# Optimization experiments

Hardware: AMD Instinct MI355X
Metric: run time of the kernel (lower is better)

Reference implementation:

```python
import jax, jax.numpy as jnp
import numpy as np
from jax import lax

B, S, D = 4, 2048, 256      # batch, seq_len, hidden_dim
F = 1024                    # ffn_dim
E = 32                      # num_experts
K = 4                       # top_k


def setup_inputs() -> dict:
    key = jax.random.key(0)
    ks = jax.random.split(key, 5)
    scale = 0.02
    x = jax.random.normal(ks[0], (B, S, D), dtype=jnp.float32)
    router_w = jax.random.normal(ks[1], (E, D), dtype=jnp.float32) * scale   # gate Linear weight [out=E, in=D]
    w_gate = jax.random.normal(ks[2], (E, F, D), dtype=jnp.float32) * scale  # per-expert [F, D]
    w_up = jax.random.normal(ks[3], (E, F, D), dtype=jnp.float32) * scale
    w_down = jax.random.normal(ks[4], (E, D, F), dtype=jnp.float32) * scale
    return {"x": x, "router_w": router_w, "w_gate": w_gate, "w_up": w_up, "w_down": w_down}


def reference(x, router_w, w_gate, w_up, w_down):
    # Eval mode: jitter noise and dropout are inactive (training-only in the source).
    b, s, d = x.shape
    T = b * s
    xf = x.reshape(T, d)                                   # [T, D]

    # --- Router ---
    logits = xf @ router_w.T                               # [T, E]
    tk_logits, tk_idx = lax.top_k(logits, K)               # [T, K]
    tk_w = jax.nn.softmax(tk_logits, axis=-1)              # [T, K]
    probs = jax.nn.softmax(logits, axis=-1)                # [T, E]
    one_hot = jax.nn.one_hot(tk_idx, E, dtype=x.dtype)     # [T, K, E]
    tokens_per_expert = one_hot.sum(axis=(0, 1))           # [E]
    f_frac = tokens_per_expert / T
    P = probs.mean(axis=0)
    aux_loss = E * (f_frac * P).sum()

    # combine[t, e] = sum_k tk_w[t,k] * [tk_idx[t,k] == e]
    combine = jnp.einsum("tk,tke->te", tk_w, one_hot)      # [T, E]

    # --- Experts: scan over experts, SwiGLU FFN, weighted accumulate ---
    def step(acc, params):
        wg, wu, wd, ce = params                            # [F,D], [F,D], [D,F], [T]
        h = jax.nn.silu(xf @ wg.T) * (xf @ wu.T)           # [T, F]
        return acc + ce[:, None] * (h @ wd.T), None

    out, _ = lax.scan(step, jnp.zeros_like(xf),
                      (w_gate, w_up, w_down, combine.T))
    return out.reshape(b, s, d), aux_loss
```

## Files before the change

kernel.cpp:

```cpp
#include <hip/hip_runtime.h>
#include <math.h>

#define TOK 8192
#define DIM 256
#define NE  32
#define NK  4
#define NF  1024

typedef __bf16 bf16x8 __attribute__((ext_vector_type(8)));
typedef float  f32x4  __attribute__((ext_vector_type(4)));
typedef unsigned short u16x8 __attribute__((ext_vector_type(8)));

__device__ __forceinline__ unsigned short f2b(float f) {
  unsigned u = __builtin_bit_cast(unsigned, f);
  unsigned r = (u + 0x7FFFu + ((u >> 16) & 1u)) >> 16;
  return (unsigned short)r;
}

__device__ __forceinline__ void gload16(const void* g, void* l) {
  __builtin_amdgcn_global_load_lds(
      (const __attribute__((address_space(1))) void*)g,
      (__attribute__((address_space(3))) void*)l, 16, 0, 0);
}

__device__ __forceinline__ void router_body(
    int bid, const float* __restrict__ x, const float* __restrict__ rw,
    int* __restrict__ counts, float* __restrict__ psum,
    int* __restrict__ etok, float* __restrict__ ewt,
    float* __restrict__ outz)
{
  __shared__ float xs[32][DIM + 4];
  __shared__ float ws[NE][DIM + 4];
  __shared__ float lg[32][NE];
  __shared__ int hist[NE];
  __shared__ int base[NE];

  const int tid = threadIdx.x;
  const int t0 = bid * 32;

  {
    float4 z4 = {0.f, 0.f, 0.f, 0.f};
    float4* og = (float4*)(outz + (size_t)t0 * DIM);
    #pragma unroll
    for (int i = 0; i < 8; i++) og[i*256 + tid] = z4;
  }

  {
    const float4* xg = (const float4*)(x + (size_t)t0 * DIM);
    for (int i = tid; i < 32 * (DIM/4); i += 256) {
      int t = i / (DIM/4), c = i % (DIM/4);
      *(float4*)&xs[t][c*4] = xg[t*(DIM/4)+c];
    }
    const float4* wgp = (const float4*)rw;
    for (int i = tid; i < NE * (DIM/4); i += 256) {
      int e = i / (DIM/4), c = i % (DIM/4);
      *(float4*)&ws[e][c*4] = wgp[e*(DIM/4)+c];
    }
  }
  if (tid < NE) hist[tid] = 0;
  __syncthreads();

  for (int i = 0; i < 4; i++) {
    int idx = i*256 + tid;
    int t = idx >> 5, e = idx & 31;
    float acc = 0.f;
    for (int c = 0; c < DIM/4; c++) {
      float4 a = *(const float4*)&xs[t][c*4];
      float4 b = *(const float4*)&ws[e][c*4];
      acc += a.x*b.x + a.y*b.y + a.z*b.z + a.w*b.w;
    }
    lg[t][e] = acc;
  }
  __syncthreads();

  int ids[NK]; int slots[NK]; float wts[NK];
  if (tid < 32) {
    const int t = tid;
    float l[NE];
    #pragma unroll
    for (int e = 0; e < NE; e++) l[e] = lg[t][e];
    unsigned mask = 0;
    float vals[NK];
    #pragma unroll
    for (int k = 0; k < NK; k++) {
      float best = -INFINITY; int bi = 0;
      for (int e = 0; e < NE; e++)
        if (!((mask >> e) & 1u) && l[e] > best) { best = l[e]; bi = e; }
      mask |= 1u << bi; vals[k] = best; ids[k] = bi;
    }
    float s4 = 0.f;
    #pragma unroll
    for (int k = 0; k < NK; k++) { wts[k] = __expf(vals[k] - vals[0]); s4 += wts[k]; }
    #pragma unroll
    for (int k = 0; k < NK; k++) wts[k] /= s4;
    float s = 0.f;
    for (int e = 0; e < NE; e++) { l[e] = __expf(l[e] - vals[0]); s += l[e]; }
    float inv = 1.f / s;
    for (int e = 0; e < NE; e++) lg[t][e] = l[e] * inv;
    #pragma unroll
    for (int k = 0; k < NK; k++) slots[k] = atomicAdd(&hist[ids[k]], 1);
  }
  __syncthreads();
  if (tid < NE) {
    float s = 0.f;
    for (int t = 0; t < 32; t++) s += lg[t][tid];
    atomicAdd(&psum[tid], s);
    int h = hist[tid];
    base[tid] = h ? atomicAdd(&counts[tid], h) : 0;
  }
  __syncthreads();
  if (tid < 32) {
    #pragma unroll
    for (int k = 0; k < NK; k++) {
      int p = base[ids[k]] + slots[k];
      etok[(size_t)ids[k]*TOK + p] = t0 + tid;
      ewt [(size_t)ids[k]*TOK + p] = wts[k];
    }
  }
}

__device__ __forceinline__ void convert_body(
    int gid, const float* __restrict__ wg_, const float* __restrict__ wu_,
    const float* __restrict__ wd_, unsigned short* __restrict__ wB)
{
  int sg  = gid >> 11;
  int idx = gid & 2047;
  int e   = sg / 48;
  int st  = sg - e * 48;
  int ch  = st / 3;
  int ty  = st - ch * 3;
  unsigned short* dst = wB + ((size_t)sg << 14);
  const float* src;
  int pos;
  if (ty < 2) {
    int f = idx >> 5, gk = idx & 31;
    const float* w = (ty == 0) ? wg_ : wu_;
    src = w + (size_t)e * (NF*DIM) + (size_t)(ch*64 + f) * DIM + (gk << 3);
    pos = f*256 + ((gk ^ (f & 7)) << 3);
  } else {
    int d = idx >> 3, fg = idx & 7;
    src = wd_ + (size_t)e * (DIM*NF) + (size_t)d * NF + (ch << 6) + (fg << 3);
    pos = (d << 6) + ((fg ^ (d & 7)) << 3);
  }
  float4 a = *(const float4*)src;
  float4 c = *(const float4*)(src + 4);
  u16x8 v;
  v[0]=f2b(a.x); v[1]=f2b(a.y); v[2]=f2b(a.z); v[3]=f2b(a.w);
  v[4]=f2b(c.x); v[5]=f2b(c.y); v[6]=f2b(c.z); v[7]=f2b(c.w);
  *(u16x8*)&dst[pos] = v;
}

__global__ __launch_bounds__(256) void fused_rc_kernel(
    const float* __restrict__ x, const float* __restrict__ rw,
    const float* __restrict__ wg_, const float* __restrict__ wu_,
    const float* __restrict__ wd_,
    int* __restrict__ counts, float* __restrict__ psum,
    int* __restrict__ etok, float* __restrict__ ewt,
    float* __restrict__ outz, unsigned short* __restrict__ wB)
{
  if (blockIdx.x < 256) {
    router_body(blockIdx.x, x, rw, counts, psum, etok, ewt, outz);
  } else {
    int gid = (blockIdx.x - 256) * 256 + threadIdx.x;
    #pragma unroll
    for (int it = 0; it < 8; it++, gid += 1536*256)
      convert_body(gid, wg_, wu_, wd_, wB);
  }
}

__global__ __launch_bounds__(256) void router_kernel(
    const float* __restrict__ x, const float* __restrict__ rw,
    int* __restrict__ counts, float* __restrict__ psum,
    int* __restrict__ etok, float* __restrict__ ewt,
    float* __restrict__ outz)
{
  router_body(blockIdx.x, x, rw, counts, psum, etok, ewt, outz);
}

__global__ void aux_kernel(const int* __restrict__ counts,
                           const float* __restrict__ psum,
                           float* __restrict__ aux_out)
{
  int tid = threadIdx.x;
  float v = 0.f;
  if (tid < NE) v = (counts[tid] / (float)TOK) * (psum[tid] / (float)TOK);
  #pragma unroll
  for (int off = 32; off; off >>= 1) v += __shfl_down(v, off);
  if (tid == 0) aux_out[0] = (float)NE * v;
}

#define PWB(N) asm volatile("s_waitcnt vmcnt(" #N ") lgkmcnt(0)\n\ts_barrier" ::: "memory")

#define ISSUE_L(sl_) do {                                               \
    const unsigned short* sp_ = wE + ((size_t)(3*c0 + (sl_)) << 14);    \
    unsigned short* dp_ = &ring[(sl_) & 3][0];                          \
    _Pragma("unroll")                                                   \
    for (int i_ = 0; i_ < 4; i_++) {                                    \
      int o_ = (i_*512 + tid) << 3;                                     \
      gload16(sp_ + o_, dp_ + o_);                                      \
    }                                                                   \
  } while (0)

#define COMP_G(rs)                                                      \
  _Pragma("unroll")                                                     \
  for (int nt = 0; nt < 2; nt++) {                                      \
    const int fl = nw*32 + nt*16 + ln;                                  \
    const int rowb = fl*256, xo = fl & 7;                               \
    ga[nt][0] = (f32x4){0,0,0,0}; ga[nt][1] = (f32x4){0,0,0,0};         \
    _Pragma("unroll")                                                   \
    for (int kk = 0; kk < 8; kk++) {                                    \
      bf16x8 bg = *(const bf16x8*)&rs[rowb + (((kk*4 + q) ^ xo) << 3)]; \
      ga[nt][0] = __builtin_amdgcn_mfma_f32_16x16x32_bf16(xf[0][kk], bg, ga[nt][0], 0,0,0); \
      ga[nt][1] = __builtin_amdgcn_mfma_f32_16x16x32_bf16(xf[1][kk], bg, ga[nt][1], 0,0,0); \
    }                                                                   \
  }

#define COMP_U(rs)                                                      \
  _Pragma("unroll")                                                     \
  for (int nt = 0; nt < 2; nt++) {                                      \
    const int fl = nw*32 + nt*16 + ln;                                  \
    const int rowb = fl*256, xo = fl & 7;                               \
    f32x4 ua0 = (f32x4){0,0,0,0}, ua1 = (f32x4){0,0,0,0};               \
    _Pragma("unroll")                                                   \
    for (int kk = 0; kk < 8; kk++) {                                    \
      bf16x8 bu = *(const bf16x8*)&rs[rowb + (((kk*4 + q) ^ xo) << 3)]; \
      ua0 = __builtin_amdgcn_mfma_f32_16x16x32_bf16(xf[0][kk], bu, ua0, 0,0,0); \
      ua1 = __builtin_amdgcn_mfma_f32_16x16x32_bf16(xf[1][kk], bu, ua1, 0,0,0); \
    }                                                                   \
    _Pragma("unroll")                                                   \
    for (int rr = 0; rr < 4; rr++) {                                    \
      float g0 = ga[nt][0][rr], g1 = ga[nt][1][rr];                     \
      hs[mw*32      + q*4 + rr][fl] = f2b((g0 / (1.f + __expf(-g0))) * ua0[rr]); \
      hs[mw*32 + 16 + q*4 + rr][fl] = f2b((g1 / (1.f + __expf(-g1))) * ua1[rr]); \
    }                                                                   \
  }

#define COMP_D(rs)                                                      \
  _Pragma("unroll")                                                     \
  for (int kk = 0; kk < 2; kk++) {                                      \
    bf16x8 a0 = *(const bf16x8*)&hs[mw*32      + ln][kk*32 + q*8];      \
    bf16x8 a1 = *(const bf16x8*)&hs[mw*32 + 16 + ln][kk*32 + q*8];      \
    _Pragma("unroll")                                                   \
    for (int nt = 0; nt < 8; nt++) {                                    \
      const int d = nw*128 + nt*16 + ln;                                \
      bf16x8 bd = *(const bf16x8*)&rs[d*64 + (((kk*4 + q) ^ (d & 7)) << 3)]; \
      oacc[nt][0] = __builtin_amdgcn_mfma_f32_16x16x32_bf16(a0, bd, oacc[nt][0], 0,0,0); \
      oacc[nt][1] = __builtin_amdgcn_mfma_f32_16x16x32_bf16(a1, bd, oacc[nt][1], 0,0,0); \
    }                                                                   \
  }

__global__ __launch_bounds__(512, 2) void expert_mfma9_kernel(
    const float* __restrict__ x,
    const unsigned short* __restrict__ wB,
    const int* __restrict__ counts,
    const int* __restrict__ etok, const float* __restrict__ ewt,
    float* __restrict__ out)
{
  __shared__ unsigned short ring[4][16384];
  __shared__ unsigned short hs[128][72];
  __shared__ int   lel[128];
  __shared__ float lwt[128];
  __shared__ int   pfx[NE + 1];

  const int tid  = threadIdx.x;
  const int lane = tid & 63;
  const int wv   = tid >> 6;
  const int mw   = wv & 3;
  const int nw   = wv >> 2;
  const int q    = lane >> 4;
  const int ln   = lane & 15;

  if (tid == 0) {
    int acc = 0;
    #pragma unroll 1
    for (int e = 0; e < NE; e++) { pfx[e] = acc; acc += (counts[e] + 127) >> 7; }
    pfx[NE] = acc;
  }
  __syncthreads();

  const int U  = __builtin_amdgcn_readfirstlane(pfx[NE] << 4);
  const int ub = ((blockIdx.x & 7) << 5) | (blockIdx.x >> 3);
  int       u  = (ub * U) >> 8;
  const int u1 = ((ub + 1) * U) >> 8;

  #pragma unroll 1
  while (u < u1) {
    const int g = u >> 4;
    int ev = 0;
    #pragma unroll 1
    while (pfx[ev + 1] <= g) ev++;
    const int e   = __builtin_amdgcn_readfirstlane(ev);
    const int t   = __builtin_amdgcn_readfirstlane(g - pfx[e]);
    const int c0  = u & 15;
    const int c1  = (16 < c0 + (u1 - u)) ? 16 : (c0 + (u1 - u));
    const int cnt = __builtin_amdgcn_readfirstlane(counts[e]);
    const int t0  = t << 7;
    const unsigned short* wE = wB + (size_t)e * 48 * 16384;
    const int*   el = etok + (size_t)e * TOK;
    const float* ew = ewt  + (size_t)e * TOK;

    if (tid < 128) {
      int gt = t0 + tid;
      lel[tid] = (gt < cnt) ? el[gt] : -1;
      lwt[tid] = (gt < cnt) ? ew[gt] : 0.f;
    }
    __syncthreads();

    bf16x8 xf[2][8];
    #pragma unroll
    for (int m = 0; m < 2; m++) {
      int row = mw*32 + m*16 + ln;
      int tok = lel[row]; if (tok < 0) tok = 0;
      const float* xr = x + (size_t)tok * DIM;
      #pragma unroll
      for (int k = 0; k < 8; k++) {
        float4 a = *(const float4*)(xr + k*32 + q*8);
        float4 c = *(const float4*)(xr + k*32 + q*8 + 4);
        union { bf16x8 v; unsigned short s[8]; } tt;
        tt.s[0]=f2b(a.x); tt.s[1]=f2b(a.y); tt.s[2]=f2b(a.z); tt.s[3]=f2b(a.w);
        tt.s[4]=f2b(c.x); tt.s[5]=f2b(c.y); tt.s[6]=f2b(c.z); tt.s[7]=f2b(c.w);
        xf[m][k] = tt.v;
      }
    }

    f32x4 oacc[8][2];
    #pragma unroll
    for (int nt = 0; nt < 8; nt++) { oacc[nt][0] = (f32x4){0,0,0,0}; oacc[nt][1] = (f32x4){0,0,0,0}; }

    const int S = 3 * (c1 - c0);

    asm volatile("s_waitcnt vmcnt(0)" ::: "memory");
    ISSUE_L(0); ISSUE_L(1); ISSUE_L(2);

    f32x4 ga[2][2];

    #pragma unroll 1
    for (int c = c0; c < c1; c++) {
      const int sb = 3 * (c - c0);
      PWB(4);
      if (sb + 3 < S) ISSUE_L(sb + 3);
      { const unsigned short* rs = ring[ sb      & 3]; COMP_G(rs); }
      { const unsigned short* rs = ring[(sb + 1) & 3]; COMP_U(rs); }
      if (sb + 3 < S) {
        PWB(4);
        ISSUE_L(sb + 4);
        ISSUE_L(sb + 5);
      } else {
        PWB(0);
      }
      { const unsigned short* rs = ring[(sb + 2) & 3]; COMP_D(rs); }
    }

    #pragma unroll
    for (int nt = 0; nt < 8; nt++) {
      int d = nw*128 + nt*16 + ln;
      #pragma unroll
      for (int m = 0; m < 2; m++)
        #pragma unroll
        for (int rr = 0; rr < 4; rr++) {
          int tl = mw*32 + m*16 + q*4 + rr;
          int tok = lel[tl];
          if (tok >= 0)
            atomicAdd(&out[(size_t)tok*DIM + d], lwt[tl] * oacc[nt][m][rr]);
        }
    }
    __syncthreads();

    u += c1 - c0;
  }
}

__global__ __launch_bounds__(512, 2) void expert_mfma5_kernel(
    const float* __restrict__ x,
    const float* __restrict__ wg_, const float* __restrict__ wu_,
    const float* __restrict__ wd_,
    const int* __restrict__ counts,
    const int* __restrict__ etok, const float* __restrict__ ewt,
    float* __restrict__ out)
{
  const int b  = blockIdx.x;
  const int j  = b >> 3;
  const int e  = (b & 7) + 8 * (j & 3);
  const int s0 = j >> 2;
  const int cnt = counts[e];

  __shared__ unsigned short stg[2][16384];
  __shared__ unsigned short hs[128][72];
  __shared__ int   lel[128];
  __shared__ float lwt[128];

  const int tid  = threadIdx.x;
  const int lane = tid & 63;
  const int wv   = tid >> 6;
  const int mw   = wv & 3;
  const int nw   = wv >> 2;
  const int q    = lane >> 4;
  const int ln   = lane & 15;

  int guOff[4], dOff[4], dRow[4], dFg[4];
  #pragma unroll
  for (int i = 0; i < 4; i++) {
    int G = i*512 + tid;
    int f = G >> 5, gk = G & 31;
    guOff[i] = f*256 + ((gk ^ (f & 7)) << 3);
    int d = G >> 3, fg = G & 7;
    dOff[i] = d*64 + ((fg ^ (d & 7)) << 3);
    dRow[i] = d; dFg[i] = fg;
  }

  const float* wgE = wg_ + (size_t)e * NF * DIM;
  const float* wuE = wu_ + (size_t)e * NF * DIM;
  const float* wdE = wd_ + (size_t)e * DIM * NF;

  const int*   el = etok + (size_t)e * TOK;
  const float* ew = ewt  + (size_t)e * TOK;

  for (int t0 = s0 * 128; t0 < cnt; t0 += 1024) {
    if (tid < 128) {
      int gt = t0 + tid;
      lel[tid] = (gt < cnt) ? el[gt] : -1;
      lwt[tid] = (gt < cnt) ? ew[gt] : 0.f;
    }
    __syncthreads();

    bf16x8 xf[2][8];
    #pragma unroll
    for (int m = 0; m < 2; m++) {
      int row = mw*32 + m*16 + ln;
      int tok = lel[row]; if (tok < 0) tok = 0;
      const float* xr = x + (size_t)tok * DIM;
      #pragma unroll
      for (int k = 0; k < 8; k++) {
        float4 a = *(const float4*)(xr + k*32 + q*8);
        float4 c = *(const float4*)(xr + k*32 + q*8 + 4);
        union { bf16x8 v; unsigned short s[8]; } t;
        t.s[0]=f2b(a.x); t.s[1]=f2b(a.y); t.s[2]=f2b(a.z); t.s[3]=f2b(a.w);
        t.s[4]=f2b(c.x); t.s[5]=f2b(c.y); t.s[6]=f2b(c.z); t.s[7]=f2b(c.w);
        xf[m][k] = t.v;
      }
    }

    f32x4 oacc[8][2];
    #pragma unroll
    for (int nt = 0; nt < 8; nt++) { oacc[nt][0] = (f32x4){0,0,0,0}; oacc[nt][1] = (f32x4){0,0,0,0}; }

    unsigned short* pA = stg[0];
    unsigned short* pB = stg[1];
    float4 r[8];

    {
      const float4* s4 = (const float4*)wgE;
      #pragma unroll
      for (int i = 0; i < 4; i++) { int G = i*512 + tid; r[2*i] = s4[2*G]; r[2*i+1] = s4[2*G+1]; }
      #pragma unroll
      for (int i = 0; i < 4; i++) {
        u16x8 v;
        v[0]=f2b(r[2*i].x);   v[1]=f2b(r[2*i].y);   v[2]=f2b(r[2*i].z);   v[3]=f2b(r[2*i].w);
        v[4]=f2b(r[2*i+1].x); v[5]=f2b(r[2*i+1].y); v[6]=f2b(r[2*i+1].z); v[7]=f2b(r[2*i+1].w);
        *(u16x8*)&pA[guOff[i]] = v;
      }
    }
    __syncthreads();

    f32x4 ga[2][2];

    for (int ch = 0; ch < 16; ch++) {
      {
        const float4* s4 = (const float4*)(wuE + (size_t)ch*16384);
        #pragma unroll
        for (int i = 0; i < 4; i++) { int G = i*512 + tid; r[2*i] = s4[2*G]; r[2*i+1] = s4[2*G+1]; }
      }
      #pragma unroll
      for (int nt = 0; nt < 2; nt++) {
        int fl = nw*32 + nt*16 + ln;
        int rowb = fl*256, xo = fl & 7;
        ga[nt][0] = (f32x4){0,0,0,0}; ga[nt][1] = (f32x4){0,0,0,0};
        #pragma unroll
        for (int kk = 0; kk < 8; kk++) {
          bf16x8 bg = *(const bf16x8*)&pA[rowb + (((kk*4 + q) ^ xo) << 3)];
          ga[nt][0] = __builtin_amdgcn_mfma_f32_16x16x32_bf16(xf[0][kk], bg, ga[nt][0], 0,0,0);
          ga[nt][1] = __builtin_amdgcn_mfma_f32_16x16x32_bf16(xf[1][kk], bg, ga[nt][1], 0,0,0);
        }
      }
      #pragma unroll
      for (int i = 0; i < 4; i++) {
        u16x8 v;
        v[0]=f2b(r[2*i].x);   v[1]=f2b(r[2*i].y);   v[2]=f2b(r[2*i].z);   v[3]=f2b(r[2*i].w);
        v[4]=f2b(r[2*i+1].x); v[5]=f2b(r[2*i+1].y); v[6]=f2b(r[2*i+1].z); v[7]=f2b(r[2*i+1].w);
        *(u16x8*)&pB[guOff[i]] = v;
      }
      __syncthreads();
      { unsigned short* t = pA; pA = pB; pB = t; }

      {
        #pragma unroll
        for (int i = 0; i < 4; i++) {
          const float4* p = (const float4*)(wdE + (size_t)dRow[i]*NF + ch*64 + dFg[i]*8);
          r[2*i] = p[0]; r[2*i+1] = p[1];
        }
      }
      #pragma unroll
      for (int nt = 0; nt < 2; nt++) {
        int fl = nw*32 + nt*16 + ln;
        int rowb = fl*256, xo = fl & 7;
        f32x4 ua0 = (f32x4){0,0,0,0}, ua1 = (f32x4){0,0,0,0};
        #pragma unroll
        for (int kk = 0; kk < 8; kk++) {
          bf16x8 bu = *(const bf16x8*)&pA[rowb + (((kk*4 + q) ^ xo) << 3)];
          ua0 = __builtin_amdgcn_mfma_f32_16x16x32_bf16(xf[0][kk], bu, ua0, 0,0,0);
          ua1 = __builtin_amdgcn_mfma_f32_16x16x32_bf16(xf[1][kk], bu, ua1, 0,0,0);
        }
        #pragma unroll
        for (int rr = 0; rr < 4; rr++) {
          float g0 = ga[nt][0][rr], g1 = ga[nt][1][rr];
          hs[mw*32      + q*4 + rr][fl] = f2b((g0 / (1.f + __expf(-g0))) * ua0[rr]);
          hs[mw*32 + 16 + q*4 + rr][fl] = f2b((g1 / (1.f + __expf(-g1))) * ua1[rr]);
        }
      }
      #pragma unroll
      for (int i = 0; i < 4; i++) {
        u16x8 v;
        v[0]=f2b(r[2*i].x);   v[1]=f2b(r[2*i].y);   v[2]=f2b(r[2*i].z);   v[3]=f2b(r[2*i].w);
        v[4]=f2b(r[2*i+1].x); v[5]=f2b(r[2*i+1].y); v[6]=f2b(r[2*i+1].z); v[7]=f2b(r[2*i+1].w);
        *(u16x8*)&pB[dOff[i]] = v;
      }
      __syncthreads();
      { unsigned short* t = pA; pA = pB; pB = t; }

      if (ch < 15) {
        const float4* s4 = (const float4*)(wgE + (size_t)(ch+1)*16384);
        #pragma unroll
        for (int i = 0; i < 4; i++) { int G = i*512 + tid; r[2*i] = s4[2*G]; r[2*i+1] = s4[2*G+1]; }
      }
      #pragma unroll
      for (int kk = 0; kk < 2; kk++) {
        bf16x8 a0 = *(const bf16x8*)&hs[mw*32      + ln][kk*32 + q*8];
        bf16x8 a1 = *(const bf16x8*)&hs[mw*32 + 16 + ln][kk*32 + q*8];
        #pragma unroll
        for (int nt = 0; nt < 8; nt++) {
          int d = nw*128 + nt*16 + ln;
          bf16x8 bd = *(const bf16x8*)&pA[d*64 + (((kk*4 + q) ^ (d & 7)) << 3)];
          oacc[nt][0] = __builtin_amdgcn_mfma_f32_16x16x32_bf16(a0, bd, oacc[nt][0], 0,0,0);
          oacc[nt][1] = __builtin_amdgcn_mfma_f32_16x16x32_bf16(a1, bd, oacc[nt][1], 0,0,0);
        }
      }
      if (ch < 15) {
        #pragma unroll
        for (int i = 0; i < 4; i++) {
          u16x8 v;
          v[0]=f2b(r[2*i].x);   v[1]=f2b(r[2*i].y);   v[2]=f2b(r[2*i].z);   v[3]=f2b(r[2*i].w);
          v[4]=f2b(r[2*i+1].x); v[5]=f2b(r[2*i+1].y); v[6]=f2b(r[2*i+1].z); v[7]=f2b(r[2*i+1].w);
          *(u16x8*)&pB[guOff[i]] = v;
        }
      }
      __syncthreads();
      { unsigned short* t = pA; pA = pB; pB = t; }
    }

    #pragma unroll
    for (int nt = 0; nt < 8; nt++) {
      int d = nw*128 + nt*16 + ln;
      #pragma unroll
      for (int m = 0; m < 2; m++)
        #pragma unroll
        for (int rr = 0; rr < 4; rr++) {
          int tl = mw*32 + m*16 + q*4 + rr;
          int tok = lel[tl];
          if (tok >= 0)
            atomicAdd(&out[(size_t)tok*DIM + d], lwt[tl] * oacc[nt][m][rr]);
        }
    }
    __syncthreads();
  }
}

extern "C" void kernel_launch(void* const* d_in, const int* in_sizes, int n_in,
                              void* d_out, int out_size, void* d_ws, size_t ws_size,
                              hipStream_t stream)
{
  const float* x  = (const float*)d_in[0];
  const float* rw = (const float*)d_in[1];
  const float* wg = (const float*)d_in[2];
  const float* wu = (const float*)d_in[3];
  const float* wd = (const float*)d_in[4];
  float* out = (float*)d_out;

  int*   counts = (int*)d_ws;
  float* psum   = (float*)((char*)d_ws + 128);
  int*   etok   = (int*)((char*)d_ws + 256);
  float* ewt    = (float*)((char*)d_ws + 256 + (size_t)NE*TOK*4);

  hipMemsetAsync(d_ws, 0, 256, stream);

  const size_t wboff = (size_t)4 << 20;
  const size_t wbsz  = (size_t)NE * 48 * 16384 * 2;
  if (ws_size >= wboff + wbsz) {
    unsigned short* wB = (unsigned short*)((char*)d_ws + wboff);
    fused_rc_kernel<<<256 + 1536, 256, 0, stream>>>(
        x, rw, wg, wu, wd, counts, psum, etok, ewt, out, wB);
    aux_kernel<<<1, 64, 0, stream>>>(counts, psum, out + (size_t)TOK*DIM);
    expert_mfma9_kernel<<<256, 512, 0, stream>>>(x, wB, counts, etok, ewt, out);
  } else {
    router_kernel<<<TOK/32, 256, 0, stream>>>(x, rw, counts, psum, etok, ewt, out);
    aux_kernel<<<1, 64, 0, stream>>>(counts, psum, out + (size_t)TOK*DIM);
    expert_mfma5_kernel<<<256, 512, 0, stream>>>(x, wg, wu, wd, counts, etok, ewt, out);
  }
}
```

Before: 325.0 us.

## Halve expert tile to 64 tokens and 32-wide F chunks, double grid occupancy

The expert kernel now processes 64-token tiles with 32-row F chunks instead of 128 tokens and 64 rows. The pre-converted bf16 weight layout is re-sliced to match, with a new XOR swizzle for the down-projection chunk and the h buffer. The LDS footprint roughly halves, so launch bounds allow 4 blocks per CU and the grid doubles to 512 blocks. This is meant to raise occupancy and balance load across experts, at the cost of less weight reuse per token and more global weight traffic.

```diff
diff --git a/kernel.cpp b/kernel.cpp
--- a/kernel.cpp
+++ b/kernel.cpp
@@ -123,24 +123,24 @@
     int gid, const float* __restrict__ wg_, const float* __restrict__ wu_,
     const float* __restrict__ wd_, unsigned short* __restrict__ wB)
 {
-  int sg  = gid >> 11;
-  int idx = gid & 2047;
-  int e   = sg / 48;
-  int st  = sg - e * 48;
+  int sg  = gid >> 10;
+  int idx = gid & 1023;
+  int e   = sg / 96;
+  int st  = sg - e * 96;
   int ch  = st / 3;
   int ty  = st - ch * 3;
-  unsigned short* dst = wB + ((size_t)sg << 14);
+  unsigned short* dst = wB + ((size_t)sg << 13);
   const float* src;
   int pos;
   if (ty < 2) {
     int f = idx >> 5, gk = idx & 31;
     const float* w = (ty == 0) ? wg_ : wu_;
-    src = w + (size_t)e * (NF*DIM) + (size_t)(ch*64 + f) * DIM + (gk << 3);
+    src = w + (size_t)e * (NF*DIM) + (size_t)(ch*32 + f) * DIM + (gk << 3);
     pos = f*256 + ((gk ^ (f & 7)) << 3);
   } else {
-    int d = idx >> 3, fg = idx & 7;
-    src = wd_ + (size_t)e * (DIM*NF) + (size_t)d * NF + (ch << 6) + (fg << 3);
-    pos = (d << 6) + ((fg ^ (d & 7)) << 3);
+    int d = idx >> 2, fg = idx & 3;
+    src = wd_ + (size_t)e * (DIM*NF) + (size_t)d * NF + (ch << 5) + (fg << 3);
+    pos = (d << 5) + ((fg ^ (d & 3)) << 3);
   }
   float4 a = *(const float4*)src;
   float4 c = *(const float4*)(src + 4);
@@ -192,74 +192,64 @@
 #define PWB(N) asm volatile("s_waitcnt vmcnt(" #N ") lgkmcnt(0)\n\ts_barrier" ::: "memory")
 
 #define ISSUE_L(sl_) do {                                               \
-    const unsigned short* sp_ = wE + ((size_t)(3*c0 + (sl_)) << 14);    \
+    const unsigned short* sp_ = wE + ((size_t)(3*c0 + (sl_)) << 13);    \
     unsigned short* dp_ = &ring[(sl_) & 3][0];                          \
     _Pragma("unroll")                                                   \
-    for (int i_ = 0; i_ < 4; i_++) {                                    \
+    for (int i_ = 0; i_ < 2; i_++) {                                    \
       int o_ = (i_*512 + tid) << 3;                                     \
       gload16(sp_ + o_, dp_ + o_);                                      \
     }                                                                   \
   } while (0)
 
 #define COMP_G(rs)                                                      \
-  _Pragma("unroll")                                                     \
-  for (int nt = 0; nt < 2; nt++) {                                      \
-    const int fl = nw*32 + nt*16 + ln;                                  \
+  { const int fl = nw*16 + ln;                                          \
     const int rowb = fl*256, xo = fl & 7;                               \
-    ga[nt][0] = (f32x4){0,0,0,0}; ga[nt][1] = (f32x4){0,0,0,0};         \
+    ga = (f32x4){0,0,0,0};                                              \
     _Pragma("unroll")                                                   \
     for (int kk = 0; kk < 8; kk++) {                                    \
       bf16x8 bg = *(const bf16x8*)&rs[rowb + (((kk*4 + q) ^ xo) << 3)]; \
-      ga[nt][0] = __builtin_amdgcn_mfma_f32_16x16x32_bf16(xf[0][kk], bg, ga[nt][0], 0,0,0); \
-      ga[nt][1] = __builtin_amdgcn_mfma_f32_16x16x32_bf16(xf[1][kk], bg, ga[nt][1], 0,0,0); \
-    }                                                                   \
-  }
+      ga = __builtin_amdgcn_mfma_f32_16x16x32_bf16(xf[kk], bg, ga, 0,0,0); \
+    } }
 
 #define COMP_U(rs)                                                      \
-  _Pragma("unroll")                                                     \
-  for (int nt = 0; nt < 2; nt++) {                                      \
-    const int fl = nw*32 + nt*16 + ln;                                  \
+  { const int fl = nw*16 + ln;                                          \
     const int rowb = fl*256, xo = fl & 7;                               \
-    f32x4 ua0 = (f32x4){0,0,0,0}, ua1 = (f32x4){0,0,0,0};               \
+    f32x4 ua = (f32x4){0,0,0,0};                                        \
     _Pragma("unroll")                                                   \
     for (int kk = 0; kk < 8; kk++) {                                    \
       bf16x8 bu = *(const bf16x8*)&rs[rowb + (((kk*4 + q) ^ xo) << 3)]; \
-      ua0 = __builtin_amdgcn_mfma_f32_16x16x32_bf16(xf[0][kk], bu, ua0, 0,0,0); \
-      ua1 = __builtin_amdgcn_mfma_f32_16x16x32_bf16(xf[1][kk], bu, ua1, 0,0,0); \
+      ua = __builtin_amdgcn_mfma_f32_16x16x32_bf16(xf[kk], bu, ua, 0,0,0); \
     }                                                                   \
+    const int fu = fl >> 3, f7 = fl & 7;                                \
     _Pragma("unroll")                                                   \
     for (int rr = 0; rr < 4; rr++) {                                    \
-      float g0 = ga[nt][0][rr], g1 = ga[nt][1][rr];                     \
-      hs[mw*32      + q*4 + rr][fl] = f2b((g0 / (1.f + __expf(-g0))) * ua0[rr]); \
-      hs[mw*32 + 16 + q*4 + rr][fl] = f2b((g1 / (1.f + __expf(-g1))) * ua1[rr]); \
-    }                                                                   \
-  }
+      const int row = mw*16 + q*4 + rr;                                 \
+      float g0 = ga[rr];                                                \
+      hs[row*32 + (((fu ^ (row & 3)) << 3) | f7)] =                     \
+          f2b((g0 / (1.f + __expf(-g0))) * ua[rr]);                     \
+    } }
 
 #define COMP_D(rs)                                                      \
-  _Pragma("unroll")                                                     \
-  for (int kk = 0; kk < 2; kk++) {                                      \
-    bf16x8 a0 = *(const bf16x8*)&hs[mw*32      + ln][kk*32 + q*8];      \
-    bf16x8 a1 = *(const bf16x8*)&hs[mw*32 + 16 + ln][kk*32 + q*8];      \
+  { const int arow = mw*16 + ln;                                        \
+    bf16x8 a = *(const bf16x8*)&hs[arow*32 + ((q ^ (arow & 3)) << 3)];  \
     _Pragma("unroll")                                                   \
     for (int nt = 0; nt < 8; nt++) {                                    \
       const int d = nw*128 + nt*16 + ln;                                \
-      bf16x8 bd = *(const bf16x8*)&rs[d*64 + (((kk*4 + q) ^ (d & 7)) << 3)]; \
-      oacc[nt][0] = __builtin_amdgcn_mfma_f32_16x16x32_bf16(a0, bd, oacc[nt][0], 0,0,0); \
-      oacc[nt][1] = __builtin_amdgcn_mfma_f32_16x16x32_bf16(a1, bd, oacc[nt][1], 0,0,0); \
-    }                                                                   \
-  }
-
-__global__ __launch_bounds__(512, 2) void expert_mfma9_kernel(
+      bf16x8 bd = *(const bf16x8*)&rs[d*32 + ((q ^ (d & 3)) << 3)];     \
+      oacc[nt] = __builtin_amdgcn_mfma_f32_16x16x32_bf16(a, bd, oacc[nt], 0,0,0); \
+    } }
+
+__global__ __launch_bounds__(512, 4) void expert_mfma10_kernel(
     const float* __restrict__ x,
     const unsigned short* __restrict__ wB,
     const int* __restrict__ counts,
     const int* __restrict__ etok, const float* __restrict__ ewt,
     float* __restrict__ out)
 {
-  __shared__ unsigned short ring[4][16384];
-  __shared__ unsigned short hs[128][72];
-  __shared__ int   lel[128];
-  __shared__ float lwt[128];
+  __shared__ unsigned short ring[4][8192];
+  __shared__ unsigned short hs[2048];
+  __shared__ int   lel[64];
+  __shared__ float lwt[64];
   __shared__ int   pfx[NE + 1];
 
   const int tid  = threadIdx.x;
@@ -273,43 +263,42 @@
   if (tid == 0) {
     int acc = 0;
     #pragma unroll 1
-    for (int e = 0; e < NE; e++) { pfx[e] = acc; acc += (counts[e] + 127) >> 7; }
+    for (int e = 0; e < NE; e++) { pfx[e] = acc; acc += (counts[e] + 63) >> 6; }
     pfx[NE] = acc;
   }
   __syncthreads();
 
-  const int U  = __builtin_amdgcn_readfirstlane(pfx[NE] << 4);
-  const int ub = ((blockIdx.x & 7) << 5) | (blockIdx.x >> 3);
-  int       u  = (ub * U) >> 8;
-  const int u1 = ((ub + 1) * U) >> 8;
+  const int U  = __builtin_amdgcn_readfirstlane(pfx[NE] << 5);
+  const int ub = ((blockIdx.x & 7) << 6) | (blockIdx.x >> 3);
+  int       u  = (ub * U) >> 9;
+  const int u1 = ((ub + 1) * U) >> 9;
 
   #pragma unroll 1
   while (u < u1) {
-    const int g = u >> 4;
+    const int g = u >> 5;
     int ev = 0;
     #pragma unroll 1
     while (pfx[ev + 1] <= g) ev++;
     const int e   = __builtin_amdgcn_readfirstlane(ev);
     const int t   = __builtin_amdgcn_readfirstlane(g - pfx[e]);
-    const int c0  = u & 15;
-    const int c1  = (16 < c0 + (u1 - u)) ? 16 : (c0 + (u1 - u));
+    const int c0  = u & 31;
+    const int c1  = (32 < c0 + (u1 - u)) ? 32 : (c0 + (u1 - u));
     const int cnt = __builtin_amdgcn_readfirstlane(counts[e]);
-    const int t0  = t << 7;
-    const unsigned short* wE = wB + (size_t)e * 48 * 16384;
+    const int t0  = t << 6;
+    const unsigned short* wE = wB + (size_t)e * 96 * 8192;
     const int*   el = etok + (size_t)e * TOK;
     const float* ew = ewt  + (size_t)e * TOK;
 
-    if (tid < 128) {
+    if (tid < 64) {
       int gt = t0 + tid;
       lel[tid] = (gt < cnt) ? el[gt] : -1;
       lwt[tid] = (gt < cnt) ? ew[gt] : 0.f;
     }
     __syncthreads();
 
-    bf16x8 xf[2][8];
-    #pragma unroll
-    for (int m = 0; m < 2; m++) {
-      int row = mw*32 + m*16 + ln;
+    bf16x8 xf[8];
+    {
+      int row = mw*16 + ln;
       int tok = lel[row]; if (tok < 0) tok = 0;
       const float* xr = x + (size_t)tok * DIM;
       #pragma unroll
@@ -319,30 +308,30 @@
         union { bf16x8 v; unsigned short s[8]; } tt;
         tt.s[0]=f2b(a.x); tt.s[1]=f2b(a.y); tt.s[2]=f2b(a.z); tt.s[3]=f2b(a.w);
         tt.s[4]=f2b(c.x); tt.s[5]=f2b(c.y); tt.s[6]=f2b(c.z); tt.s[7]=f2b(c.w);
-        xf[m][k] = tt.v;
-      }
-    }
-
-    f32x4 oacc[8][2];
-    #pragma unroll
-    for (int nt = 0; nt < 8; nt++) { oacc[nt][0] = (f32x4){0,0,0,0}; oacc[nt][1] = (f32x4){0,0,0,0}; }
+        xf[k] = tt.v;
+      }
+    }
+
+    f32x4 oacc[8];
+    #pragma unroll
+    for (int nt = 0; nt < 8; nt++) oacc[nt] = (f32x4){0,0,0,0};
 
     const int S = 3 * (c1 - c0);
 
     asm volatile("s_waitcnt vmcnt(0)" ::: "memory");
     ISSUE_L(0); ISSUE_L(1); ISSUE_L(2);
 
-    f32x4 ga[2][2];
+    f32x4 ga;
 
     #pragma unroll 1
     for (int c = c0; c < c1; c++) {
       const int sb = 3 * (c - c0);
-      PWB(4);
+      PWB(2);
       if (sb + 3 < S) ISSUE_L(sb + 3);
       { const unsigned short* rs = ring[ sb      & 3]; COMP_G(rs); }
       { const unsigned short* rs = ring[(sb + 1) & 3]; COMP_U(rs); }
       if (sb + 3 < S) {
-        PWB(4);
+        PWB(2);
         ISSUE_L(sb + 4);
         ISSUE_L(sb + 5);
       } else {
@@ -355,14 +344,12 @@
     for (int nt = 0; nt < 8; nt++) {
       int d = nw*128 + nt*16 + ln;
       #pragma unroll
-      for (int m = 0; m < 2; m++)
-        #pragma unroll
-        for (int rr = 0; rr < 4; rr++) {
-          int tl = mw*32 + m*16 + q*4 + rr;
-          int tok = lel[tl];
-          if (tok >= 0)
-            atomicAdd(&out[(size_t)tok*DIM + d], lwt[tl] * oacc[nt][m][rr]);
-        }
+      for (int rr = 0; rr < 4; rr++) {
+        int tl = mw*16 + q*4 + rr;
+        int tok = lel[tl];
+        if (tok >= 0)
+          atomicAdd(&out[(size_t)tok*DIM + d], lwt[tl] * oacc[nt][rr]);
+      }
     }
     __syncthreads();
 
@@ -385,7 +372,7 @@
   const int cnt = counts[e];
 
   __shared__ unsigned short stg[2][16384];
-  __shared__ unsigned short hs[128][72];
+  __shared__ unsigned short hsf[128][72];
   __shared__ int   lel[128];
   __shared__ float lwt[128];
 
@@ -513,8 +500,8 @@
         #pragma unroll
         for (int rr = 0; rr < 4; rr++) {
           float g0 = ga[nt][0][rr], g1 = ga[nt][1][rr];
-          hs[mw*32      + q*4 + rr][fl] = f2b((g0 / (1.f + __expf(-g0))) * ua0[rr]);
-          hs[mw*32 + 16 + q*4 + rr][fl] = f2b((g1 / (1.f + __expf(-g1))) * ua1[rr]);
+          hsf[mw*32      + q*4 + rr][fl] = f2b((g0 / (1.f + __expf(-g0))) * ua0[rr]);
+          hsf[mw*32 + 16 + q*4 + rr][fl] = f2b((g1 / (1.f + __expf(-g1))) * ua1[rr]);
         }
       }
       #pragma unroll
@@ -534,8 +521,8 @@
       }
       #pragma unroll
       for (int kk = 0; kk < 2; kk++) {
-        bf16x8 a0 = *(const bf16x8*)&hs[mw*32      + ln][kk*32 + q*8];
-        bf16x8 a1 = *(const bf16x8*)&hs[mw*32 + 16 + ln][kk*32 + q*8];
+        bf16x8 a0 = *(const bf16x8*)&hsf[mw*32      + ln][kk*32 + q*8];
+        bf16x8 a1 = *(const bf16x8*)&hsf[mw*32 + 16 + ln][kk*32 + q*8];
         #pragma unroll
         for (int nt = 0; nt < 8; nt++) {
           int d = nw*128 + nt*16 + ln;
@@ -593,13 +580,13 @@
   hipMemsetAsync(d_ws, 0, 256, stream);
 
   const size_t wboff = (size_t)4 << 20;
-  const size_t wbsz  = (size_t)NE * 48 * 16384 * 2;
+  const size_t wbsz  = (size_t)NE * 96 * 8192 * 2;
   if (ws_size >= wboff + wbsz) {
     unsigned short* wB = (unsigned short*)((char*)d_ws + wboff);
     fused_rc_kernel<<<256 + 1536, 256, 0, stream>>>(
         x, rw, wg, wu, wd, counts, psum, etok, ewt, out, wB);
     aux_kernel<<<1, 64, 0, stream>>>(counts, psum, out + (size_t)TOK*DIM);
-    expert_mfma9_kernel<<<256, 512, 0, stream>>>(x, wB, counts, etok, ewt, out);
+    expert_mfma10_kernel<<<512, 512, 0, stream>>>(x, wB, counts, etok, ewt, out);
   } else {
     router_kernel<<<TOK/32, 256, 0, stream>>>(x, rw, counts, psum, etok, ewt, out);
     aux_kernel<<<1, 64, 0, stream>>>(counts, psum, out + (size_t)TOK*DIM);
```

Measured after the change: 317.1 us. 2.4% less time.
